# Performance work log

Hardware: AMD Instinct MI355X
Metric: run time of the kernel (lower is better)

The kernel has to match this reference:

```python
import jax, jax.numpy as jnp
import numpy as np

EPS = 1e-5
DEPTH = 3
NQ = 12


def _bn(x, g, b):
    # BatchNorm1d in training mode: batch statistics, biased variance
    mu = x.mean(0)
    var = x.var(0)
    return (x - mu) / jnp.sqrt(var + EPS) * g + b


def _ln(x, g, b):
    mu = x.mean(-1, keepdims=True)
    var = x.var(-1, keepdims=True)
    return (x - mu) / jnp.sqrt(var + EPS) * g + b


def _apply_1q(s, U, q):
    # s: [B, 2^NQ] complex; U: [2,2] (shared) or [B,2,2] (per-sample); qubit q = q-th MSB
    B = s.shape[0]
    s = s.reshape(B, 2 ** q, 2, -1)
    sub = 'ij,bajc->baic' if U.ndim == 2 else 'bij,bajc->baic'
    return jnp.einsum(sub, U, s).reshape(B, -1)


def _apply_cry(s, theta, c):
    # controlled-Ry(theta): control qubit c, target qubit c+1 (adjacent)
    B = s.shape[0]
    s = s.reshape(B, 2 ** c, 2, 2, -1)
    co = jnp.cos(theta / 2).astype(s.dtype)
    si = jnp.sin(theta / 2).astype(s.dtype)
    s1 = s[:, :, 1]  # control = |1> block
    new1 = jnp.stack([co * s1[:, :, 0] - si * s1[:, :, 1],
                      si * s1[:, :, 0] + co * s1[:, :, 1]], axis=2)
    s = jnp.concatenate([s[:, :, :1], new1[:, :, None]], axis=2)
    return s.reshape(B, -1)


def _measure(s):
    # P(qubit q measures |1>) for each qubit
    p = jnp.abs(s) ** 2  # [B, 2^NQ]
    B = p.shape[0]
    probs = [p.reshape(B, 2 ** q, 2, -1).sum(axis=(1, 3))[:, 1] for q in range(NQ)]
    return jnp.stack(probs, axis=1)  # [B, NQ]


def _rot_mats(rot):
    # fused Rz(rz) @ Ry(ry) @ Rx(rx) for each (depth, qubit) -> [DEPTH, NQ, 2, 2]
    hx, hy, hz = rot[..., 0] / 2, rot[..., 1] / 2, rot[..., 2] / 2
    cx, sx = jnp.cos(hx), jnp.sin(hx)
    Rx = jnp.stack([jnp.stack([cx + 0j, -1j * sx], -1),
                    jnp.stack([-1j * sx, cx + 0j], -1)], -2)
    cy, sy = jnp.cos(hy), jnp.sin(hy)
    Ry = jnp.stack([jnp.stack([cy, -sy], -1),
                    jnp.stack([sy, cy], -1)], -2).astype(jnp.complex64)
    ez = jnp.exp(-1j * hz)
    z0 = jnp.zeros_like(ez)
    Rz = jnp.stack([jnp.stack([ez, z0], -1),
                    jnp.stack([z0, jnp.conj(ez)], -1)], -2)
    return jnp.einsum('...ij,...jk,...kl->...il', Rz, Ry, Rx).astype(jnp.complex64)


def _quantum_layer(x, We, be, gi, bi, rot, ent, Wd, bd, go, bo):
    e = jnp.tanh(_bn(x @ We.T + be, gi, bi))  # [B, NQ]
    nrm = jnp.linalg.norm(e, axis=1, keepdims=True)
    a = jnp.where(nrm > 0, e / nrm, e)        # per-sample L2-normalized amplitudes
    B = x.shape[0]
    s = jnp.zeros((B, 2 ** NQ), jnp.complex64).at[:, 0].set(1.0)
    # amplitude encoding: Ry(2*arcsin(|a|)) then phase pi (sign) if a<0 -> diag(1,-1)@Ry
    ang = 2.0 * jnp.arcsin(jnp.clip(jnp.abs(a), 0.0, 1.0))
    c, si = jnp.cos(ang / 2), jnp.sin(ang / 2)
    sg = jnp.where(a < 0, -1.0, 1.0)
    for q in range(NQ):
        U = jnp.stack([jnp.stack([c[:, q], -si[:, q]], -1),
                       jnp.stack([sg[:, q] * si[:, q], sg[:, q] * c[:, q]], -1)],
                      -2).astype(jnp.complex64)  # [B,2,2]
        s = _apply_1q(s, U, q)
    # parameterized circuit: per-qubit fused Rz.Ry.Rx, then nearest-neighbor CRy chain
    U = _rot_mats(rot)
    for d in range(DEPTH):
        for q in range(NQ):
            s = _apply_1q(s, U[d, q], q)
        for i in range(NQ - 1):
            s = _apply_cry(s, ent[d, i], i)
    m = _measure(s)
    return _bn(m @ Wd.T + bd, go, bo)


def setup_inputs() -> dict:
    key = jax.random.key(0)
    ks = jax.random.split(key, 16)
    B, IN, H1, H2, H3, OUT = 512, 512, 512, 512, 1024, 256

    def lin(k, o, i):
        k1, k2 = jax.random.split(k)
        lim = 1.0 / np.sqrt(i)
        return (jax.random.uniform(k1, (o, i), jnp.float32, -lim, lim),
                jax.random.uniform(k2, (o,), jnp.float32, -lim, lim))

    qWe0, qbe0 = lin(ks[1], NQ, IN)
    qWd0, qbd0 = lin(ks[2], H1, NQ)
    qWe1, qbe1 = lin(ks[3], NQ, H1)
    qWd1, qbd1 = lin(ks[4], H2, NQ)
    W2, b2 = lin(ks[5], H3, H2)
    Wo, bo = lin(ks[6], OUT, H3)
    return {
        'x': jax.random.normal(ks[0], (B, IN), jnp.float32),
        'qWe0': qWe0, 'qbe0': qbe0,
        'qgi0': jnp.ones(NQ), 'qbi0': jnp.zeros(NQ),
        'rot0': 0.1 * jax.random.normal(ks[7], (DEPTH, NQ, 3), jnp.float32),
        'ent0': 0.1 * jax.random.normal(ks[8], (DEPTH, NQ - 1), jnp.float32),
        'qWd0': qWd0, 'qbd0': qbd0,
        'qgo0': jnp.ones(H1), 'qbo0': jnp.zeros(H1),
        'qWe1': qWe1, 'qbe1': qbe1,
        'qgi1': jnp.ones(NQ), 'qbi1': jnp.zeros(NQ),
        'rot1': 0.1 * jax.random.normal(ks[9], (DEPTH, NQ, 3), jnp.float32),
        'ent1': 0.1 * jax.random.normal(ks[10], (DEPTH, NQ - 1), jnp.float32),
        'qWd1': qWd1, 'qbd1': qbd1,
        'qgo1': jnp.ones(H2), 'qbo1': jnp.zeros(H2),
        'W2': W2, 'b2': b2, 'ln2g': jnp.ones(H3), 'ln2b': jnp.zeros(H3),
        'Wo': Wo, 'bo': bo, 'lnog': jnp.ones(OUT), 'lnob': jnp.zeros(OUT),
    }


def reference(x, qWe0, qbe0, qgi0, qbi0, rot0, ent0, qWd0, qbd0, qgo0, qbo0,
              qWe1, qbe1, qgi1, qbi1, rot1, ent1, qWd1, qbd1, qgo1, qbo1,
              W2, b2, ln2g, ln2b, Wo, bo, lnog, lnob):
    h = _quantum_layer(x, qWe0, qbe0, qgi0, qbi0, rot0, ent0, qWd0, qbd0, qgo0, qbo0)
    h = _quantum_layer(h, qWe1, qbe1, qgi1, qbi1, rot1, ent1, qWd1, qbd1, qgo1, qbo1)
    h = jax.nn.relu(_ln(h @ W2.T + b2, ln2g, ln2b))  # classical block (dropout = identity, eval)
    return _ln(h @ Wo.T + bo, lnog, lnob)
```

## Files before the change

kernel.cpp:

```cpp
#include <hip/hip_runtime.h>
#include <math.h>

#define EPS   1e-5f
#define NQ    12
#define DEPTH 3
#define BATCH 512
#define DIM   4096

__device__ inline float2 cmul(float2 a, float2 b) {
    return make_float2(a.x*b.x - a.y*b.y, a.x*b.y + a.y*b.x);
}
__device__ inline float2 cmac2(float2 ua, float2 s, float2 ub, float2 p) {
    return make_float2(ua.x*s.x - ua.y*s.y + ub.x*p.x - ub.y*p.y,
                       ua.x*s.y + ua.y*s.x + ub.x*p.y + ub.y*p.x);
}

__device__ inline int swz(int a) { return a ^ ((a >> 4) & 15); }

template<int HB> __device__ inline int ampl8(int t, int k) {
    return ((t >> HB) << (HB+3)) | (k << HB) | (t & ((1<<HB)-1));
}

template<int FHB, int THB>
__device__ inline void remap8(float2* amp, float2* lds2, int t) {
    #pragma unroll
    for (int k = 0; k < 8; ++k) lds2[swz(ampl8<FHB>(t, k))] = amp[k];
    __syncthreads();
    #pragma unroll
    for (int k = 0; k < 8; ++k) amp[k] = lds2[swz(ampl8<THB>(t, k))];
    __syncthreads();
}

template<int BP>
__device__ inline void one_q8(float2* amp, float2 u00, float2 u01, float2 u10, float2 u11) {
    #pragma unroll
    for (int g = 0; g < 4; ++g) {
        const int j0 = ((g >> BP) << (BP+1)) | (g & ((1<<BP)-1));
        const int j1 = j0 | (1 << BP);
        float2 a0 = amp[j0], a1 = amp[j1];
        amp[j0] = cmac2(u00, a0, u01, a1);
        amp[j1] = cmac2(u10, a0, u11, a1);
    }
}

template<int CB, int TB>
__device__ inline void cry8(float2* amp, float co, float si) {
    #pragma unroll
    for (int m = 0; m < 8; ++m) {
        if (((m >> CB) & 1) && !((m >> TB) & 1)) {
            const int j1 = m | (1 << TB);
            float2 a0 = amp[m], a1 = amp[j1];
            amp[m]  = make_float2(co*a0.x - si*a1.x, co*a0.y - si*a1.y);
            amp[j1] = make_float2(si*a0.x + co*a1.x, si*a0.y + co*a1.y);
        }
    }
}

__device__ void consts_body(int t,
        const float* rot0, const float* ent0, const float* rot1, const float* ent1,
        float2* Uc, float2* Cc) {
    if (t < 72) {
        int layer = t / 36, rem = t % 36, d = rem / 12, q = rem % 12;
        const float* rot = layer ? rot1 : rot0;
        float hx = 0.5f * rot[(d*NQ + q)*3 + 0];
        float hy = 0.5f * rot[(d*NQ + q)*3 + 1];
        float hz = 0.5f * rot[(d*NQ + q)*3 + 2];
        float cx = cosf(hx), sx = sinf(hx);
        float cy = cosf(hy), sy = sinf(hy);
        float2 m00 = make_float2( cy*cx,  sy*sx);
        float2 m01 = make_float2(-sy*cx, -cy*sx);
        float2 m10 = make_float2( sy*cx, -cy*sx);
        float2 m11 = make_float2( cy*cx, -sy*sx);
        float2 ez  = make_float2(cosf(hz), -sinf(hz));
        float2 ezc = make_float2(ez.x, -ez.y);
        float2* U = Uc + t*4;
        U[0] = cmul(ez,  m00);
        U[1] = cmul(ez,  m01);
        U[2] = cmul(ezc, m10);
        U[3] = cmul(ezc, m11);
    } else if (t < 72 + 66) {
        int idx = t - 72, layer = idx / 33, rem = idx % 33;
        const float* ent = layer ? ent1 : ent0;
        float th = 0.5f * ent[rem];
        Cc[idx] = make_float2(cosf(th), sinf(th));
    }
}

__global__ __launch_bounds__(256) void encode0_consts_kernel(
        const float* __restrict__ X, const float* __restrict__ We,
        const float* __restrict__ be, float* __restrict__ Yraw,
        const float* __restrict__ rot0, const float* __restrict__ ent0,
        const float* __restrict__ rot1, const float* __restrict__ ent1,
        float2* __restrict__ Uc, float2* __restrict__ Cc) {
    int tid = threadIdx.x;
    if (blockIdx.x == 128) {
        consts_body(tid, rot0, ent0, rot1, ent1, Uc, Cc);
        return;
    }
    __shared__ float w[NQ][512];
    {
        const float4* src = (const float4*)We;
        float4* dst = (float4*)&w[0][0];
        #pragma unroll
        for (int i = tid; i < NQ*128; i += 256) dst[i] = src[i];
    }
    __syncthreads();
    int wave = tid >> 6, lane = tid & 63;
    int b = blockIdx.x * 4 + wave;
    const float4* xr = (const float4*)(X + (size_t)b * 512);
    float acc[NQ] = {};
    #pragma unroll
    for (int j = 0; j < 2; ++j) {
        float4 xv = xr[lane + 64*j];
        #pragma unroll
        for (int q = 0; q < NQ; ++q) {
            float4 wv = ((const float4*)&w[q][0])[lane + 64*j];
            acc[q] += xv.x*wv.x + xv.y*wv.y + xv.z*wv.z + xv.w*wv.w;
        }
    }
    #pragma unroll
    for (int q = 0; q < NQ; ++q) {
        float v = acc[q];
        #pragma unroll
        for (int off = 32; off; off >>= 1) v += __shfl_xor(v, off);
        if (lane == q) Yraw[b*NQ + q] = v + be[q];
    }
}

__global__ __launch_bounds__(512, 4) void qsim8_kernel(
        const float* __restrict__ Yraw, const float* __restrict__ gi,
        const float* __restrict__ bi, const float2* __restrict__ UcAll,
        const float2* __restrict__ CcAll, int layer,
        float* __restrict__ mout, float* __restrict__ zeroY) {
    int blk = blockIdx.x, t = threadIdx.x;
    const float2* Uc = UcAll + layer * DEPTH * NQ * 4;
    const float2* Cc = CcAll + layer * DEPTH * (NQ - 1);
    __shared__ float2 lds2[DIM];
    __shared__ float sred[192];
    if (zeroY && t < NQ) zeroY[blk*NQ + t] = 0.f;

    float sum[NQ], sq[NQ];
    {
        const float4* Y4 = (const float4*)Yraw;
        float4 va = Y4[t*3+0], vb = Y4[t*3+1], vc = Y4[t*3+2];
        float r[12] = {va.x,va.y,va.z,va.w, vb.x,vb.y,vb.z,vb.w, vc.x,vc.y,vc.z,vc.w};
        #pragma unroll
        for (int q = 0; q < NQ; ++q) { sum[q] = r[q]; sq[q] = r[q]*r[q]; }
    }
    int lane = t & 63, wave = t >> 6;
    #pragma unroll
    for (int q = 0; q < NQ; ++q) {
        #pragma unroll
        for (int off = 32; off; off >>= 1) {
            sum[q] += __shfl_xor(sum[q], off);
            sq[q]  += __shfl_xor(sq[q],  off);
        }
    }
    if (lane == 0) {
        #pragma unroll
        for (int q = 0; q < NQ; ++q) {
            sred[wave*24 + q]      = sum[q];
            sred[wave*24 + 12 + q] = sq[q];
        }
    }
    __syncthreads();
    float a[NQ]; float n2 = 0.f;
    const float* yr = Yraw + blk*NQ;
    #pragma unroll
    for (int q = 0; q < NQ; ++q) {
        float s = 0.f, s2 = 0.f;
        #pragma unroll
        for (int w8 = 0; w8 < 8; ++w8) { s += sred[w8*24 + q]; s2 += sred[w8*24 + 12 + q]; }
        float mu  = s  * (1.f/512.f);
        float var = s2 * (1.f/512.f) - mu*mu;
        float val = (yr[q] - mu) * rsqrtf(var + EPS) * gi[q] + bi[q];
        a[q] = tanhf(val);
        n2 += a[q]*a[q];
    }
    float scn = (n2 > 0.f) ? rsqrtf(n2) : 1.f;
    #pragma unroll
    for (int q = 0; q < NQ; ++q) a[q] *= scn;

    float2 v0[NQ], v1[NQ];
    #pragma unroll
    for (int q = 0; q < NQ; ++q) {
        float sv = fminf(fabsf(a[q]), 1.f);
        float c  = sqrtf(fmaxf(1.f - sv*sv, 0.f));
        float ss = (a[q] < 0.f) ? -sv : sv;
        const float2* U = Uc + q*4;
        v0[q] = make_float2(U[0].x*c + U[1].x*ss, U[0].y*c + U[1].y*ss);
        v1[q] = make_float2(U[2].x*c + U[3].x*ss, U[2].y*c + U[3].y*ss);
    }
    float2 common = make_float2(1.f, 0.f);
    #pragma unroll
    for (int j = 0; j < 9; ++j)
        common = cmul(common, ((t >> j) & 1) ? v1[11-j] : v0[11-j]);
    float2 amp[8];
    amp[0] = common;
    #pragma unroll
    for (int m = 0; m < 3; ++m) {
        const int q = 2 - m;
        #pragma unroll
        for (int k = 0; k < (1<<m); ++k) {
            amp[k | (1<<m)] = cmul(amp[k], v1[q]);
            amp[k]          = cmul(amp[k], v0[q]);
        }
    }

    for (int d = 0; d < DEPTH; ++d) {
        const float2* Ud = Uc + d*NQ*4;
        const float2* Cd = Cc + d*(NQ-1);
        if (d > 0) {
            one_q8<2>(amp, Ud[0],  Ud[1],  Ud[2],  Ud[3]);
            one_q8<1>(amp, Ud[4],  Ud[5],  Ud[6],  Ud[7]);
            one_q8<0>(amp, Ud[8],  Ud[9],  Ud[10], Ud[11]);
        }
        cry8<2,1>(amp, Cd[0].x, Cd[0].y);
        cry8<1,0>(amp, Cd[1].x, Cd[1].y);
        remap8<9,7>(amp, lds2, t);
        if (d > 0) {
            one_q8<1>(amp, Ud[12], Ud[13], Ud[14], Ud[15]);
            one_q8<0>(amp, Ud[16], Ud[17], Ud[18], Ud[19]);
        }
        cry8<2,1>(amp, Cd[2].x, Cd[2].y);
        cry8<1,0>(amp, Cd[3].x, Cd[3].y);
        remap8<7,5>(amp, lds2, t);
        if (d > 0) {
            one_q8<1>(amp, Ud[20], Ud[21], Ud[22], Ud[23]);
            one_q8<0>(amp, Ud[24], Ud[25], Ud[26], Ud[27]);
        }
        cry8<2,1>(amp, Cd[4].x, Cd[4].y);
        cry8<1,0>(amp, Cd[5].x, Cd[5].y);
        remap8<5,3>(amp, lds2, t);
        if (d > 0) {
            one_q8<1>(amp, Ud[28], Ud[29], Ud[30], Ud[31]);
            one_q8<0>(amp, Ud[32], Ud[33], Ud[34], Ud[35]);
        }
        cry8<2,1>(amp, Cd[6].x, Cd[6].y);
        cry8<1,0>(amp, Cd[7].x, Cd[7].y);
        remap8<3,1>(amp, lds2, t);
        if (d > 0) {
            one_q8<1>(amp, Ud[36], Ud[37], Ud[38], Ud[39]);
            one_q8<0>(amp, Ud[40], Ud[41], Ud[42], Ud[43]);
        }
        cry8<2,1>(amp, Cd[8].x, Cd[8].y);
        cry8<1,0>(amp, Cd[9].x, Cd[9].y);
        remap8<1,0>(amp, lds2, t);
        if (d > 0) {
            one_q8<0>(amp, Ud[44], Ud[45], Ud[46], Ud[47]);
        }
        cry8<1,0>(amp, Cd[10].x, Cd[10].y);
        if (d < DEPTH-1) remap8<0,9>(amp, lds2, t);
    }

    float msum = 0.f, p9 = 0.f, p10 = 0.f, p11 = 0.f;
    #pragma unroll
    for (int k = 0; k < 8; ++k) {
        float m = amp[k].x*amp[k].x + amp[k].y*amp[k].y;
        msum += m;
        if (k & 4) p9  += m;
        if (k & 2) p10 += m;
        if (k & 1) p11 += m;
    }
    #pragma unroll
    for (int q = 0; q < NQ; ++q) {
        float v;
        if (q < 9)        v = ((t >> (8-q)) & 1) ? msum : 0.f;
        else if (q == 9)  v = p9;
        else if (q == 10) v = p10;
        else              v = p11;
        #pragma unroll
        for (int off = 32; off; off >>= 1) v += __shfl_xor(v, off);
        if (lane == 0) sred[q*8 + wave] = v;
    }
    __syncthreads();
    if (t < NQ) {
        float r = 0.f;
        #pragma unroll
        for (int w8 = 0; w8 < 8; ++w8) r += sred[t*8 + w8];
        mout[blk*NQ + t] = r;
    }
}

__global__ __launch_bounds__(512) void decode_kernel(
        const float* __restrict__ m, const float* __restrict__ Wd,
        const float* __restrict__ bd, const float* __restrict__ go,
        const float* __restrict__ bo, float* __restrict__ outT) {
    int h = blockIdx.x, b = threadIdx.x;
    __shared__ float sm[BATCH * 13];
    __shared__ float2 red[8];
    const float4* m4 = (const float4*)m;
    for (int f4 = b; f4 < 1536; f4 += 512) {
        float4 v = m4[f4];
        int base = f4*4; int row = base/12; int q = base - row*12;
        float* dst = sm + row*13 + q;
        dst[0]=v.x; dst[1]=v.y; dst[2]=v.z; dst[3]=v.w;
    }
    __syncthreads();
    float z = bd[h];
    #pragma unroll
    for (int q = 0; q < NQ; ++q) z += sm[b*13 + q] * Wd[h*NQ + q];
    float2 v = make_float2(z, z*z);
    int lane = b & 63, wave = b >> 6;
    for (int off = 32; off; off >>= 1) { v.x += __shfl_down(v.x, off); v.y += __shfl_down(v.y, off); }
    if (lane == 0) red[wave] = v;
    __syncthreads();
    float s = 0.f, s2 = 0.f;
    #pragma unroll
    for (int wv = 0; wv < 8; ++wv) { s += red[wv].x; s2 += red[wv].y; }
    float mu  = s  * (1.f/512.f);
    float var = s2 * (1.f/512.f) - mu*mu;
    outT[(size_t)h*BATCH + b] = (z - mu) * rsqrtf(var + EPS) * go[h] + bo[h];
}

__global__ __launch_bounds__(256) void encode1_kernel(
        const float* __restrict__ h1T, const float* __restrict__ We,
        const float* __restrict__ be, float* __restrict__ Yraw1) {
    __shared__ float w[NQ][512];
    __shared__ float red[4*64*NQ];
    int tid = threadIdx.x, blk = blockIdx.x;
    {
        const float4* src = (const float4*)We;
        float4* dst = (float4*)&w[0][0];
        #pragma unroll
        for (int i = tid; i < NQ*128; i += 256) dst[i] = src[i];
    }
    __syncthreads();
    int kc = blk >> 3, bc = blk & 7;
    int bl = tid & 63, hg = tid >> 6;
    int b = bc*64 + bl;
    float acc[NQ] = {};
    #pragma unroll
    for (int i = 0; i < 8; ++i) {
        int h = kc*32 + hg*8 + i;
        float xv = h1T[(size_t)h*512 + b];
        #pragma unroll
        for (int q = 0; q < NQ; ++q) acc[q] += xv * w[q][h];
    }
    #pragma unroll
    for (int q = 0; q < NQ; ++q) red[(hg*64 + bl)*NQ + q] = acc[q];
    __syncthreads();
    for (int i = tid; i < 64*NQ; i += 256) {
        int bl2 = i / NQ, q = i - bl2*NQ;
        float v = red[bl2*NQ+q] + red[(64+bl2)*NQ+q] + red[(128+bl2)*NQ+q] + red[(192+bl2)*NQ+q];
        if (kc == 0) v += be[q];
        atomicAdd(&Yraw1[(size_t)(bc*64 + bl2)*NQ + q], v);
    }
}

__global__ __launch_bounds__(256) void gemm1_kernel(
        const float* __restrict__ AT, const float* __restrict__ W,
        float* __restrict__ Cpart) {
    __shared__ float As[2][32][64];
    __shared__ float Bs[2][32][68];
    const int b0 = blockIdx.x * 64, j0 = blockIdx.y * 64;
    const int kbase = blockIdx.z * 128;
    float* C = Cpart + (size_t)blockIdx.z * 512 * 1024;
    const int tid = threadIdx.x;
    const int tr = tid >> 4, tc = tid & 15;
    const int a_kk = tid >> 4, a_f4 = tid & 15;
    const int b_jj = tid >> 3, b_k4 = (tid & 7) * 4;
    float4 ra0, ra1, rb0, rb1;
    float acc[4][4] = {};
    {
        const int k0 = kbase;
        ra0 = *(const float4*)(AT + (size_t)(k0 + a_kk)*512 + b0 + a_f4*4);
        ra1 = *(const float4*)(AT + (size_t)(k0 + a_kk + 16)*512 + b0 + a_f4*4);
        rb0 = *(const float4*)(W + (size_t)(j0 + b_jj)*512 + k0 + b_k4);
        rb1 = *(const float4*)(W + (size_t)(j0 + b_jj + 32)*512 + k0 + b_k4);
        *(float4*)&As[0][a_kk][a_f4*4] = ra0;
        *(float4*)&As[0][a_kk+16][a_f4*4] = ra1;
        Bs[0][b_k4+0][b_jj] = rb0.x; Bs[0][b_k4+1][b_jj] = rb0.y;
        Bs[0][b_k4+2][b_jj] = rb0.z; Bs[0][b_k4+3][b_jj] = rb0.w;
        Bs[0][b_k4+0][b_jj+32] = rb1.x; Bs[0][b_k4+1][b_jj+32] = rb1.y;
        Bs[0][b_k4+2][b_jj+32] = rb1.z; Bs[0][b_k4+3][b_jj+32] = rb1.w;
    }
    __syncthreads();
    for (int s = 0; s < 4; ++s) {
        if (s < 3) {
            const int k0 = kbase + (s+1)*32;
            ra0 = *(const float4*)(AT + (size_t)(k0 + a_kk)*512 + b0 + a_f4*4);
            ra1 = *(const float4*)(AT + (size_t)(k0 + a_kk + 16)*512 + b0 + a_f4*4);
            rb0 = *(const float4*)(W + (size_t)(j0 + b_jj)*512 + k0 + b_k4);
            rb1 = *(const float4*)(W + (size_t)(j0 + b_jj + 32)*512 + k0 + b_k4);
        }
        const int bf = s & 1;
        #pragma unroll
        for (int kk = 0; kk < 32; ++kk) {
            float4 a  = *(const float4*)&As[bf][kk][tr*4];
            float4 bv = *(const float4*)&Bs[bf][kk][tc*4];
            acc[0][0] += a.x*bv.x; acc[0][1] += a.x*bv.y; acc[0][2] += a.x*bv.z; acc[0][3] += a.x*bv.w;
            acc[1][0] += a.y*bv.x; acc[1][1] += a.y*bv.y; acc[1][2] += a.y*bv.z; acc[1][3] += a.y*bv.w;
            acc[2][0] += a.z*bv.x; acc[2][1] += a.z*bv.y; acc[2][2] += a.z*bv.z; acc[2][3] += a.z*bv.w;
            acc[3][0] += a.w*bv.x; acc[3][1] += a.w*bv.y; acc[3][2] += a.w*bv.z; acc[3][3] += a.w*bv.w;
        }
        if (s < 3) {
            const int nb = bf ^ 1;
            *(float4*)&As[nb][a_kk][a_f4*4] = ra0;
            *(float4*)&As[nb][a_kk+16][a_f4*4] = ra1;
            Bs[nb][b_k4+0][b_jj] = rb0.x; Bs[nb][b_k4+1][b_jj] = rb0.y;
            Bs[nb][b_k4+2][b_jj] = rb0.z; Bs[nb][b_k4+3][b_jj] = rb0.w;
            Bs[nb][b_k4+0][b_jj+32] = rb1.x; Bs[nb][b_k4+1][b_jj+32] = rb1.y;
            Bs[nb][b_k4+2][b_jj+32] = rb1.z; Bs[nb][b_k4+3][b_jj+32] = rb1.w;
        }
        __syncthreads();
    }
    #pragma unroll
    for (int r = 0; r < 4; ++r) {
        float4 o = make_float4(acc[r][0], acc[r][1], acc[r][2], acc[r][3]);
        *(float4*)(C + (size_t)(b0 + tr*4 + r)*1024 + j0 + tc*4) = o;
    }
}

__global__ __launch_bounds__(256) void ln_relu_kernel(
        const float* __restrict__ P, const float* __restrict__ bias,
        const float* __restrict__ g, const float* __restrict__ be,
        float* __restrict__ Y) {
    int b = blockIdx.x, tid = threadIdx.x;
    __shared__ float2 red[4];
    float v[4];
    #pragma unroll
    for (int j = 0; j < 4; ++j) {
        int col = tid + j*256;
        float t = bias[col];
        #pragma unroll
        for (int z = 0; z < 4; ++z) t += P[(size_t)z*524288 + (size_t)b*1024 + col];
        v[j] = t;
    }
    float2 r = make_float2(v[0]+v[1]+v[2]+v[3],
                           v[0]*v[0]+v[1]*v[1]+v[2]*v[2]+v[3]*v[3]);
    int lane = tid & 63, wave = tid >> 6;
    for (int off = 32; off; off >>= 1) { r.x += __shfl_down(r.x, off); r.y += __shfl_down(r.y, off); }
    if (lane == 0) red[wave] = r;
    __syncthreads();
    float s = red[0].x + red[1].x + red[2].x + red[3].x;
    float s2 = red[0].y + red[1].y + red[2].y + red[3].y;
    float mu  = s  * (1.f/1024.f);
    float var = s2 * (1.f/1024.f) - mu*mu;
    float inv = rsqrtf(var + EPS);
    float* yr = Y + (size_t)b * 1024;
    #pragma unroll
    for (int j = 0; j < 4; ++j) {
        int col = tid + j*256;
        yr[col] = fmaxf((v[j]-mu)*inv*g[col] + be[col], 0.f);
    }
}

__global__ __launch_bounds__(256) void gemm2_kernel(
        const float* __restrict__ Amat, const float* __restrict__ W,
        float* __restrict__ Cpart) {
    __shared__ __align__(16) char smem[27000];
    float (*As)[32][36] = (float(*)[32][36])smem;
    float (*Bs)[32][68] = (float(*)[32][68])(smem + 9216);
    const int b0 = blockIdx.x * 32, j0 = blockIdx.y * 64;
    const int kbase = blockIdx.z * 128;
    float* C = Cpart + (size_t)blockIdx.z * 512 * 256;
    const int tid = threadIdx.x;
    const int tr = tid >> 4, tc = tid & 15;
    const int l_r = tid >> 3, l_k4 = (tid & 7) * 4;
    float4 ra0, rb0, rb1;
    float acc[2][4] = {};
    {
        const int k0 = kbase;
        ra0 = *(const float4*)(Amat + (size_t)(b0 + l_r)*1024 + k0 + l_k4);
        rb0 = *(const float4*)(W + (size_t)(j0 + l_r)*1024 + k0 + l_k4);
        rb1 = *(const float4*)(W + (size_t)(j0 + l_r + 32)*1024 + k0 + l_k4);
        As[0][l_k4+0][l_r] = ra0.x; As[0][l_k4+1][l_r] = ra0.y;
        As[0][l_k4+2][l_r] = ra0.z; As[0][l_k4+3][l_r] = ra0.w;
        Bs[0][l_k4+0][l_r] = rb0.x; Bs[0][l_k4+1][l_r] = rb0.y;
        Bs[0][l_k4+2][l_r] = rb0.z; Bs[0][l_k4+3][l_r] = rb0.w;
        Bs[0][l_k4+0][l_r+32] = rb1.x; Bs[0][l_k4+1][l_r+32] = rb1.y;
        Bs[0][l_k4+2][l_r+32] = rb1.z; Bs[0][l_k4+3][l_r+32] = rb1.w;
    }
    __syncthreads();
    for (int s = 0; s < 4; ++s) {
        if (s < 3) {
            const int k0 = kbase + (s+1)*32;
            ra0 = *(const float4*)(Amat + (size_t)(b0 + l_r)*1024 + k0 + l_k4);
            rb0 = *(const float4*)(W + (size_t)(j0 + l_r)*1024 + k0 + l_k4);
            rb1 = *(const float4*)(W + (size_t)(j0 + l_r + 32)*1024 + k0 + l_k4);
        }
        const int bf = s & 1;
        #pragma unroll
        for (int kk = 0; kk < 32; ++kk) {
            float a0 = As[bf][kk][tr*2], a1 = As[bf][kk][tr*2+1];
            float4 bv = *(const float4*)&Bs[bf][kk][tc*4];
            acc[0][0] += a0*bv.x; acc[0][1] += a0*bv.y; acc[0][2] += a0*bv.z; acc[0][3] += a0*bv.w;
            acc[1][0] += a1*bv.x; acc[1][1] += a1*bv.y; acc[1][2] += a1*bv.z; acc[1][3] += a1*bv.w;
        }
        if (s < 3) {
            const int nb = bf ^ 1;
            As[nb][l_k4+0][l_r] = ra0.x; As[nb][l_k4+1][l_r] = ra0.y;
            As[nb][l_k4+2][l_r] = ra0.z; As[nb][l_k4+3][l_r] = ra0.w;
            Bs[nb][l_k4+0][l_r] = rb0.x; Bs[nb][l_k4+1][l_r] = rb0.y;
            Bs[nb][l_k4+2][l_r] = rb0.z; Bs[nb][l_k4+3][l_r] = rb0.w;
            Bs[nb][l_k4+0][l_r+32] = rb1.x; Bs[nb][l_k4+1][l_r+32] = rb1.y;
            Bs[nb][l_k4+2][l_r+32] = rb1.z; Bs[nb][l_k4+3][l_r+32] = rb1.w;
        }
        __syncthreads();
    }
    #pragma unroll
    for (int r = 0; r < 2; ++r) {
        float4 o = make_float4(acc[r][0], acc[r][1], acc[r][2], acc[r][3]);
        *(float4*)(C + (size_t)(b0 + tr*2 + r)*256 + j0 + tc*4) = o;
    }
}

__global__ __launch_bounds__(256) void ln_out_kernel(
        const float* __restrict__ P, const float* __restrict__ bias,
        const float* __restrict__ g, const float* __restrict__ be,
        float* __restrict__ Y) {
    int b = blockIdx.x, tid = threadIdx.x;
    __shared__ float2 red[4];
    float v0 = bias[tid];
    #pragma unroll
    for (int z = 0; z < 8; ++z) v0 += P[(size_t)z*131072 + (size_t)b*256 + tid];
    float2 v = make_float2(v0, v0*v0);
    int lane = tid & 63, wave = tid >> 6;
    for (int off = 32; off; off >>= 1) { v.x += __shfl_down(v.x, off); v.y += __shfl_down(v.y, off); }
    if (lane == 0) red[wave] = v;
    __syncthreads();
    float s = red[0].x + red[1].x + red[2].x + red[3].x;
    float s2 = red[0].y + red[1].y + red[2].y + red[3].y;
    float mu  = s  * (1.f/256.f);
    float var = s2 * (1.f/256.f) - mu*mu;
    Y[(size_t)b*256 + tid] = (v0 - mu) * rsqrtf(var + EPS) * g[tid] + be[tid];
}

extern "C" void kernel_launch(void* const* d_in, const int* in_sizes, int n_in,
                              void* d_out, int out_size, void* d_ws, size_t ws_size,
                              hipStream_t stream) {
    const float* x    = (const float*)d_in[0];
    const float* qWe0 = (const float*)d_in[1];
    const float* qbe0 = (const float*)d_in[2];
    const float* qgi0 = (const float*)d_in[3];
    const float* qbi0 = (const float*)d_in[4];
    const float* rot0 = (const float*)d_in[5];
    const float* ent0 = (const float*)d_in[6];
    const float* qWd0 = (const float*)d_in[7];
    const float* qbd0 = (const float*)d_in[8];
    const float* qgo0 = (const float*)d_in[9];
    const float* qbo0 = (const float*)d_in[10];
    const float* qWe1 = (const float*)d_in[11];
    const float* qbe1 = (const float*)d_in[12];
    const float* qgi1 = (const float*)d_in[13];
    const float* qbi1 = (const float*)d_in[14];
    const float* rot1 = (const float*)d_in[15];
    const float* ent1 = (const float*)d_in[16];
    const float* qWd1 = (const float*)d_in[17];
    const float* qbd1 = (const float*)d_in[18];
    const float* qgo1 = (const float*)d_in[19];
    const float* qbo1 = (const float*)d_in[20];
    const float* W2   = (const float*)d_in[21];
    const float* b2   = (const float*)d_in[22];
    const float* ln2g = (const float*)d_in[23];
    const float* ln2b = (const float*)d_in[24];
    const float* Wo   = (const float*)d_in[25];
    const float* bo   = (const float*)d_in[26];
    const float* lnog = (const float*)d_in[27];
    const float* lnob = (const float*)d_in[28];
    float* out = (float*)d_out;
    float* ws  = (float*)d_ws;

    float2* Uc   = (float2*)ws;
    float2* Cc   = Uc + 288;
    float* Yraw0 = ws + 1024;
    float* m0    = ws + 7680;
    float* Yraw1 = ws + 14336;
    float* m1    = ws + 20992;
    float* h1T   = ws + 65536;
    float* h2T   = ws + 589824;
    float* t3p   = ws + 851968;
    float* t3n   = ws + 2949120;
    float* t4p   = ws + 3473408;

    hipLaunchKernelGGL(encode0_consts_kernel, dim3(129), dim3(256), 0, stream,
                       x, qWe0, qbe0, Yraw0, rot0, ent0, rot1, ent1, Uc, Cc);
    hipLaunchKernelGGL(qsim8_kernel, dim3(512), dim3(512), 0, stream,
                       Yraw0, qgi0, qbi0, Uc, Cc, 0, m0, Yraw1);
    hipLaunchKernelGGL(decode_kernel, dim3(512), dim3(512), 0, stream,
                       m0, qWd0, qbd0, qgo0, qbo0, h1T);
    hipLaunchKernelGGL(encode1_kernel, dim3(128), dim3(256), 0, stream,
                       h1T, qWe1, qbe1, Yraw1);
    hipLaunchKernelGGL(qsim8_kernel, dim3(512), dim3(512), 0, stream,
                       Yraw1, qgi1, qbi1, Uc, Cc, 1, m1, (float*)nullptr);
    hipLaunchKernelGGL(decode_kernel, dim3(512), dim3(512), 0, stream,
                       m1, qWd1, qbd1, qgo1, qbo1, h2T);
    hipLaunchKernelGGL(gemm1_kernel, dim3(8, 16, 4), dim3(256), 0, stream,
                       h2T, W2, t3p);
    hipLaunchKernelGGL(ln_relu_kernel, dim3(512), dim3(256), 0, stream,
                       t3p, b2, ln2g, ln2b, t3n);
    hipLaunchKernelGGL(gemm2_kernel, dim3(16, 4, 8), dim3(256), 0, stream,
                       t3n, Wo, t4p);
    hipLaunchKernelGGL(ln_out_kernel, dim3(512), dim3(256), 0, stream,
                       t4p, bo, lnog, lnob, out);
}
```

Measured before the change: 235.7 us.

## Cut LDS remaps per depth in statevector sim by handling cross-window CRY

The qubit-window schedule in the state-vector kernel moves from sliding windows that overlap by one qubit (five LDS remaps per depth) to windows that advance three qubits at a time (four remaps per depth). The CRY gate that straddles two windows is applied through a new per-thread select gate, which uses the control bit taken from the thread index to choose between the rotation and the identity. The aim is fewer shared-memory exchanges and barriers per depth. In exchange every thread pays for the selected gate even when its control bit is zero.

```diff
diff --git a/kernel.cpp b/kernel.cpp
--- a/kernel.cpp
+++ b/kernel.cpp
@@ -52,6 +52,21 @@
             float2 a0 = amp[m], a1 = amp[j1];
             amp[m]  = make_float2(co*a0.x - si*a1.x, co*a0.y - si*a1.y);
             amp[j1] = make_float2(si*a0.x + co*a1.x, si*a0.y + co*a1.y);
+        }
+    }
+}
+
+template<int TB>
+__device__ inline void crysel8(float2* amp, int ctrl, float co, float si) {
+    float co2 = ctrl ? co : 1.f;
+    float s2  = ctrl ? si : 0.f;
+    #pragma unroll
+    for (int m = 0; m < 8; ++m) {
+        if (!((m >> TB) & 1)) {
+            const int j1 = m | (1 << TB);
+            float2 a0 = amp[m], a1 = amp[j1];
+            amp[m]  = make_float2(co2*a0.x - s2*a1.x, co2*a0.y - s2*a1.y);
+            amp[j1] = make_float2(s2*a0.x + co2*a1.x, s2*a0.y + co2*a1.y);
         }
     }
 }
@@ -127,7 +142,7 @@
     }
 }
 
-__global__ __launch_bounds__(512, 4) void qsim8_kernel(
+__global__ __launch_bounds__(512, 4) void qsim4w_kernel(
         const float* __restrict__ Yraw, const float* __restrict__ gi,
         const float* __restrict__ bi, const float2* __restrict__ UcAll,
         const float2* __restrict__ CcAll, int layer,
@@ -198,12 +213,12 @@
     float2 amp[8];
     amp[0] = common;
     #pragma unroll
-    for (int m = 0; m < 3; ++m) {
-        const int q = 2 - m;
-        #pragma unroll
-        for (int k = 0; k < (1<<m); ++k) {
-            amp[k | (1<<m)] = cmul(amp[k], v1[q]);
-            amp[k]          = cmul(amp[k], v0[q]);
+    for (int mb = 0; mb < 3; ++mb) {
+        const int qb = 2 - mb;
+        #pragma unroll
+        for (int k = 0; k < (1<<mb); ++k) {
+            amp[k | (1<<mb)] = cmul(amp[k], v1[qb]);
+            amp[k]           = cmul(amp[k], v0[qb]);
         }
     }
 
@@ -217,38 +232,32 @@
         }
         cry8<2,1>(amp, Cd[0].x, Cd[0].y);
         cry8<1,0>(amp, Cd[1].x, Cd[1].y);
-        remap8<9,7>(amp, lds2, t);
+        remap8<9,6>(amp, lds2, t);
         if (d > 0) {
-            one_q8<1>(amp, Ud[12], Ud[13], Ud[14], Ud[15]);
-            one_q8<0>(amp, Ud[16], Ud[17], Ud[18], Ud[19]);
-        }
-        cry8<2,1>(amp, Cd[2].x, Cd[2].y);
-        cry8<1,0>(amp, Cd[3].x, Cd[3].y);
-        remap8<7,5>(amp, lds2, t);
+            one_q8<2>(amp, Ud[12], Ud[13], Ud[14], Ud[15]);
+            one_q8<1>(amp, Ud[16], Ud[17], Ud[18], Ud[19]);
+            one_q8<0>(amp, Ud[20], Ud[21], Ud[22], Ud[23]);
+        }
+        crysel8<2>(amp, (t >> 6) & 1, Cd[2].x, Cd[2].y);
+        cry8<2,1>(amp, Cd[3].x, Cd[3].y);
+        cry8<1,0>(amp, Cd[4].x, Cd[4].y);
+        remap8<6,3>(amp, lds2, t);
         if (d > 0) {
-            one_q8<1>(amp, Ud[20], Ud[21], Ud[22], Ud[23]);
-            one_q8<0>(amp, Ud[24], Ud[25], Ud[26], Ud[27]);
-        }
-        cry8<2,1>(amp, Cd[4].x, Cd[4].y);
-        cry8<1,0>(amp, Cd[5].x, Cd[5].y);
-        remap8<5,3>(amp, lds2, t);
-        if (d > 0) {
+            one_q8<2>(amp, Ud[24], Ud[25], Ud[26], Ud[27]);
             one_q8<1>(amp, Ud[28], Ud[29], Ud[30], Ud[31]);
             one_q8<0>(amp, Ud[32], Ud[33], Ud[34], Ud[35]);
         }
+        crysel8<2>(amp, (t >> 3) & 1, Cd[5].x, Cd[5].y);
         cry8<2,1>(amp, Cd[6].x, Cd[6].y);
         cry8<1,0>(amp, Cd[7].x, Cd[7].y);
-        remap8<3,1>(amp, lds2, t);
+        remap8<3,0>(amp, lds2, t);
         if (d > 0) {
-            one_q8<1>(amp, Ud[36], Ud[37], Ud[38], Ud[39]);
-            one_q8<0>(amp, Ud[40], Ud[41], Ud[42], Ud[43]);
-        }
-        cry8<2,1>(amp, Cd[8].x, Cd[8].y);
-        cry8<1,0>(amp, Cd[9].x, Cd[9].y);
-        remap8<1,0>(amp, lds2, t);
-        if (d > 0) {
+            one_q8<2>(amp, Ud[36], Ud[37], Ud[38], Ud[39]);
+            one_q8<1>(amp, Ud[40], Ud[41], Ud[42], Ud[43]);
             one_q8<0>(amp, Ud[44], Ud[45], Ud[46], Ud[47]);
         }
+        crysel8<2>(amp, t & 1, Cd[8].x, Cd[8].y);
+        cry8<2,1>(amp, Cd[9].x,  Cd[9].y);
         cry8<1,0>(amp, Cd[10].x, Cd[10].y);
         if (d < DEPTH-1) remap8<0,9>(amp, lds2, t);
     }
@@ -576,13 +585,13 @@
 
     hipLaunchKernelGGL(encode0_consts_kernel, dim3(129), dim3(256), 0, stream,
                        x, qWe0, qbe0, Yraw0, rot0, ent0, rot1, ent1, Uc, Cc);
-    hipLaunchKernelGGL(qsim8_kernel, dim3(512), dim3(512), 0, stream,
+    hipLaunchKernelGGL(qsim4w_kernel, dim3(512), dim3(512), 0, stream,
                        Yraw0, qgi0, qbi0, Uc, Cc, 0, m0, Yraw1);
     hipLaunchKernelGGL(decode_kernel, dim3(512), dim3(512), 0, stream,
                        m0, qWd0, qbd0, qgo0, qbo0, h1T);
     hipLaunchKernelGGL(encode1_kernel, dim3(128), dim3(256), 0, stream,
                        h1T, qWe1, qbe1, Yraw1);
-    hipLaunchKernelGGL(qsim8_kernel, dim3(512), dim3(512), 0, stream,
+    hipLaunchKernelGGL(qsim4w_kernel, dim3(512), dim3(512), 0, stream,
                        Yraw1, qgi1, qbi1, Uc, Cc, 1, m1, (float*)nullptr);
     hipLaunchKernelGGL(decode_kernel, dim3(512), dim3(512), 0, stream,
                        m1, qWd1, qbd1, qgo1, qbo1, h2T);
```

Result: faster. 230.6 us (-2.2%).
